# Kernel tuning notes

Measured on AMD Instinct MI355X. Metric: run time of the kernel, lower is better.

## Reference

```python
import jax, jax.numpy as jnp
import numpy as np

B, T, V, H = 16, 128, 32000, 768
P = H // 2
NBOW = 64
PAD = 0
EPS = 0.05     # label smoothing
TAU = 0.07
W_CE, W_AL, W_BOW, W_DIV, W_VAR = 1.0, 0.5, 0.2, 0.1, 0.05
BOW_IDS = jnp.arange(NBOW, dtype=jnp.int32) * 500  # registered buffer bow_indices_tensor


def _ln(x, g, b):
    m = jnp.mean(x, axis=-1, keepdims=True)
    v = jnp.mean((x - m) ** 2, axis=-1, keepdims=True)
    return (x - m) / jnp.sqrt(v + 1e-5) * g + b


def _l2norm(x):
    return x / jnp.maximum(jnp.linalg.norm(x, axis=-1, keepdims=True), 1e-12)


def _proj(x, g, bn, W1, b1, W2, b2):
    h = _ln(x, g, bn)
    h = jax.nn.gelu(h @ W1 + b1, approximate=False)  # torch nn.GELU default = exact
    return h @ W2 + b2


def setup_inputs() -> dict:
    key = jax.random.key(0)
    ks = jax.random.split(key, 12)
    s = 0.02
    return {
        "logits": jax.random.normal(ks[0], (B, T, V), dtype=jnp.float32),
        "labels": jax.random.randint(ks[1], (B, T), 0, V, dtype=jnp.int32),
        "attention_mask": jnp.ones((B, T), dtype=jnp.int32),
        "encoder_features": jax.random.normal(ks[2], (B, H), dtype=jnp.float32),
        "decoder_hidden": jax.random.normal(ks[3], (B, T, H), dtype=jnp.float32),
        "ln_g_e": jnp.ones((H,), jnp.float32), "ln_b_e": jnp.zeros((H,), jnp.float32),
        "W1_e": jax.random.normal(ks[4], (H, P), jnp.float32) * s, "b1_e": jnp.zeros((P,), jnp.float32),
        "W2_e": jax.random.normal(ks[5], (P, P), jnp.float32) * s, "b2_e": jnp.zeros((P,), jnp.float32),
        "ln_g_t": jnp.ones((H,), jnp.float32), "ln_b_t": jnp.zeros((H,), jnp.float32),
        "W1_t": jax.random.normal(ks[6], (H, P), jnp.float32) * s, "b1_t": jnp.zeros((P,), jnp.float32),
        "W2_t": jax.random.normal(ks[7], (P, P), jnp.float32) * s, "b2_t": jnp.zeros((P,), jnp.float32),
        "W_bow": jax.random.normal(ks[8], (H, NBOW), jnp.float32) * s, "b_bow": jnp.zeros((NBOW,), jnp.float32),
    }


def _forward(logits, labels, attention_mask, encoder_features, decoder_hidden,
             ln_g_e, ln_b_e, W1_e, b1_e, W2_e, b2_e,
             ln_g_t, ln_b_t, W1_t, b1_t, W2_t, b2_t,
             W_bow, b_bow):
    # --- label-smoothed CE over valid (non-pad, non -100) tokens ---
    valid = (labels != PAD) & (labels != -100)                      # (B,T)
    lab = jnp.clip(labels, 0, V - 1)
    lp = jax.nn.log_softmax(logits, axis=-1)                        # (B,T,V)
    lp_lab = jnp.take_along_axis(lp, lab[..., None], axis=-1)[..., 0]
    tok_loss = -((1.0 - EPS) * lp_lab + (EPS / V) * lp.sum(-1))     # smooth target = (1-eps) at label + eps/V everywhere
    vf = valid.astype(jnp.float32)
    ce = (tok_loss * vf).sum() / jnp.maximum(vf.sum(), 1.0)

    # --- contrastive alignment (InfoNCE both ways) ---
    m = attention_mask[..., None].astype(jnp.float32)               # (B,T,1)
    pooled = (decoder_hidden * m).sum(1) / jnp.maximum(m.sum(1), 1.0)
    z_e = _l2norm(_proj(encoder_features, ln_g_e, ln_b_e, W1_e, b1_e, W2_e, b2_e))
    z_t = _l2norm(_proj(pooled, ln_g_t, ln_b_t, W1_t, b1_t, W2_t, b2_t))
    sim = (z_e @ z_t.T) / TAU                                       # (B,B)
    li = -jnp.diag(jax.nn.log_softmax(sim, axis=-1)).mean()
    lj = -jnp.diag(jax.nn.log_softmax(sim.T, axis=-1)).mean()
    align = 0.5 * (li + lj)

    # --- BoW BCE: target[b,i] = any valid token of row b equals bow id i ---
    match = (lab[:, :, None] == BOW_IDS[None, None, :]) & valid[:, :, None]
    bow_t = match.any(axis=1).astype(jnp.float32)                   # (B,NBOW)
    bl = encoder_features @ W_bow + b_bow
    bce = jnp.mean(jnp.maximum(bl, 0.0) - bl * bow_t + jnp.log1p(jnp.exp(-jnp.abs(bl))))

    # --- diversity: mean |off-diagonal cosine sim| of encoder features ---
    nf = _l2norm(encoder_features)
    sm = nf @ nf.T
    off = 1.0 - jnp.eye(B, dtype=jnp.float32)
    div = (jnp.abs(sm) * off).sum() / (B * B - B)

    # --- variance: mean exp(-var_dim) (torch.var uses ddof=1) ---
    fvar = jnp.var(encoder_features, axis=0, ddof=1)
    var_l = jnp.mean(jnp.exp(-fvar))

    return W_CE * ce + W_AL * align + W_BOW * bce + W_DIV * div + W_VAR * var_l


def reference(logits, labels, attention_mask, encoder_features, decoder_hidden,
              ln_g_e, ln_b_e, W1_e, b1_e, W2_e, b2_e,
              ln_g_t, ln_b_t, W1_t, b1_t, W2_t, b2_t,
              W_bow, b_bow):
    return _forward(logits, labels, attention_mask, encoder_features, decoder_hidden,
                    ln_g_e, ln_b_e, W1_e, b1_e, W2_e, b2_e,
                    ln_g_t, ln_b_t, W1_t, b1_t, W2_t, b2_t,
                    W_bow, b_bow)
```

## Files before the change

### kernel.cpp

```cpp
#include <hip/hip_runtime.h>
#include <math.h>

#define BB 16
#define TT 128
#define VV 32000
#define HH 768
#define PP 384
#define NBOWD 64
#define EPS_LS 0.05f
#define TAUC 0.07f
#define SMALLB 101

__device__ __forceinline__ float blockReduceSum256(float v, float* sh) {
  int tid = threadIdx.x;
  sh[tid] = v;
  __syncthreads();
  for (int s = 128; s > 0; s >>= 1) {
    if (tid < s) sh[tid] += sh[tid + s];
    __syncthreads();
  }
  float r = sh[0];
  __syncthreads();
  return r;
}

__global__ __launch_bounds__(256) void fused_main(
    const float* __restrict__ logits, const int* __restrict__ labels, const int* __restrict__ amask,
    const float* __restrict__ enc, const float* __restrict__ dh,
    const float* __restrict__ g_e, const float* __restrict__ be_, const float* __restrict__ W1e,
    const float* __restrict__ b1e, const float* __restrict__ W2e, const float* __restrict__ b2e,
    const float* __restrict__ g_t, const float* __restrict__ bt_, const float* __restrict__ W1t,
    const float* __restrict__ b1t, const float* __restrict__ W2t, const float* __restrict__ b2t,
    const float* __restrict__ W_bow, const float* __restrict__ b_bow,
    float* __restrict__ tok, float* __restrict__ vfs,
    float* __restrict__ ze, float* __restrict__ zt,
    float* __restrict__ bowp, float* __restrict__ divp, float* __restrict__ var_p) {
  __shared__ float smem[1792];
  int tid = threadIdx.x;
  int blk = blockIdx.x;

  if (blk >= SMALLB) {
    int row = blk - SMALLB;
    const float* x = logits + (size_t)row * VV;
    const float4* x4 = (const float4*)x;
    float sa0 = 0.f, sa1 = 0.f, sa2 = 0.f, sa3 = 0.f;
    float ta0 = 0.f, ta1 = 0.f, ta2 = 0.f, ta3 = 0.f;
#pragma unroll
    for (int grp = 0; grp < 3; ++grp) {
      float4 v[8];
      const int base = (grp << 11) + tid;
#pragma unroll
      for (int u = 0; u < 8; ++u) v[u] = x4[base + (u << 8)];
#pragma unroll
      for (int u = 0; u < 8; ++u) {
        float4 w = v[u];
        float e = (__expf(w.x) + __expf(w.y)) + (__expf(w.z) + __expf(w.w));
        float q = (w.x + w.y) + (w.z + w.w);
        if ((u & 3) == 0) { sa0 += e; ta0 += q; }
        else if ((u & 3) == 1) { sa1 += e; ta1 += q; }
        else if ((u & 3) == 2) { sa2 += e; ta2 += q; }
        else { sa3 += e; ta3 += q; }
      }
    }
    {
      float4 v[7];
      const int base = 6144 + tid;
#pragma unroll
      for (int u = 0; u < 7; ++u) v[u] = x4[base + (u << 8)];
#pragma unroll
      for (int u = 0; u < 7; ++u) {
        float4 w = v[u];
        float e = (__expf(w.x) + __expf(w.y)) + (__expf(w.z) + __expf(w.w));
        float q = (w.x + w.y) + (w.z + w.w);
        if ((u & 3) == 0) { sa0 += e; ta0 += q; }
        else if ((u & 3) == 1) { sa1 += e; ta1 += q; }
        else if ((u & 3) == 2) { sa2 += e; ta2 += q; }
        else { sa3 += e; ta3 += q; }
      }
    }
    if (tid < 64) {
      float4 w = x4[7936 + tid];
      sa3 += (__expf(w.x) + __expf(w.y)) + (__expf(w.z) + __expf(w.w));
      ta3 += (w.x + w.y) + (w.z + w.w);
    }
    float s = (sa0 + sa1) + (sa2 + sa3);
    float sx = (ta0 + ta1) + (ta2 + ta3);

    float* ss_ = smem;
    float* sxa = smem + 256;
    ss_[tid] = s; sxa[tid] = sx;
    __syncthreads();
    for (int o = 128; o > 0; o >>= 1) {
      if (tid < o) {
        ss_[tid] += ss_[tid + o];
        sxa[tid] += sxa[tid + o];
      }
      __syncthreads();
    }
    if (tid == 0) {
      float L = logf(ss_[0]), SX = sxa[0];
      int lab = labels[row];
      bool valid = (lab != 0) && (lab != -100);
      int lc = lab < 0 ? 0 : (lab > VV - 1 ? VV - 1 : lab);
      float xl = x[lc];
      float lp_lab = xl - L;
      float lp_sum = SX - (float)VV * L;
      float tl = -((1.f - EPS_LS) * lp_lab + (EPS_LS / (float)VV) * lp_sum);
      tok[row] = valid ? tl : 0.f;
      vfs[row] = valid ? 1.f : 0.f;
    }
    return;
  }

  if (blk < 32) {
    float* xs = smem;
    float* hs = smem + 768;
    float* red = smem + 1152;
    float* mf = smem + 1408;
    float* mden = smem + 1536;
    bool is_t = blk >= BB;
    int b = blk & (BB - 1);
    const float *g, *bb_, *W1, *b1, *W2, *b2;
    float* zout;
    if (is_t) { g = g_t; bb_ = bt_; W1 = W1t; b1 = b1t; W2 = W2t; b2 = b2t; zout = zt; }
    else      { g = g_e; bb_ = be_; W1 = W1e; b1 = b1e; W2 = W2e; b2 = b2e; zout = ze; }

    if (is_t) {
      if (tid < TT) mf[tid] = (float)amask[b * TT + tid];
      __syncthreads();
      if (tid == 0) {
        float sum = 0.f;
        for (int t = 0; t < TT; t++) sum += mf[t];
        mden[0] = fmaxf(sum, 1.f);
      }
      __syncthreads();
      const float* dbase = dh + (size_t)b * TT * HH;
      for (int h = tid; h < HH; h += 256) {
        const float* db = dbase + h;
        float a0 = 0.f, a1 = 0.f, a2 = 0.f, a3 = 0.f;
#pragma unroll 8
        for (int t = 0; t < TT; t += 4) {
          a0 += db[(t + 0) * HH] * mf[t + 0];
          a1 += db[(t + 1) * HH] * mf[t + 1];
          a2 += db[(t + 2) * HH] * mf[t + 2];
          a3 += db[(t + 3) * HH] * mf[t + 3];
        }
        xs[h] = ((a0 + a1) + (a2 + a3)) / mden[0];
      }
    } else {
      for (int k = tid; k < HH; k += 256) xs[k] = enc[b * HH + k];
    }
    __syncthreads();

    float s1 = 0.f, s2 = 0.f;
    for (int k = tid; k < HH; k += 256) { float v = xs[k]; s1 += v; s2 += v * v; }
    s1 = blockReduceSum256(s1, red);
    s2 = blockReduceSum256(s2, red);
    float mean = s1 / (float)HH;
    float var = s2 / (float)HH - mean * mean;
    float rstd = rsqrtf(var + 1e-5f);
    for (int k = tid; k < HH; k += 256) xs[k] = (xs[k] - mean) * rstd * g[k] + bb_[k];
    __syncthreads();

    for (int j = tid; j < PP; j += 256) {
      float a0 = 0.f, a1 = 0.f;
#pragma unroll 8
      for (int k = 0; k < HH; k += 2) {
        a0 += xs[k] * W1[k * PP + j];
        a1 += xs[k + 1] * W1[(k + 1) * PP + j];
      }
      float acc = b1[j] + a0 + a1;
      hs[j] = 0.5f * acc * (1.f + erff(acc * 0.70710678118654752440f));
    }
    __syncthreads();
    for (int j = tid; j < PP; j += 256) {
      float a0 = 0.f, a1 = 0.f;
#pragma unroll 8
      for (int k = 0; k < PP; k += 2) {
        a0 += hs[k] * W2[k * PP + j];
        a1 += hs[k + 1] * W2[(k + 1) * PP + j];
      }
      xs[j] = b2[j] + a0 + a1;
    }
    __syncthreads();
    float sq = 0.f;
    for (int j = tid; j < PP; j += 256) { float v = xs[j]; sq += v * v; }
    sq = blockReduceSum256(sq, red);
    float inv = 1.f / fmaxf(sqrtf(sq), 1e-12f);
    for (int j = tid; j < PP; j += 256) zout[b * PP + j] = xs[j] * inv;
    return;
  }

  if (blk < 96) {
    int bb = blk - 32;
    int b = bb >> 2, kq = bb & 3;
    int iw = tid & 63, ks = tid >> 6;
    const float* er = enc + b * HH;
    int k0 = kq * 192 + ks * 48;
    float acc = 0.f;
#pragma unroll 8
    for (int k = 0; k < 48; ++k) acc += er[k0 + k] * W_bow[(k0 + k) * NBOWD + iw];
    smem[ks * 64 + iw] = acc;
    __syncthreads();
    if (tid < 64) bowp[bb * 64 + tid] = smem[tid] + smem[64 + tid] + smem[128 + tid] + smem[192 + tid];
    return;
  }

  if (blk < 100) {
    int kq = blk - 96;
    int i = tid >> 4, j = tid & 15;
    const float* a = enc + i * HH + kq * 192;
    const float* c = enc + j * HH + kq * 192;
    float a0 = 0.f, a1 = 0.f;
#pragma unroll 8
    for (int k = 0; k < 192; k += 2) {
      a0 += a[k] * c[k];
      a1 += a[k + 1] * c[k + 1];
    }
    divp[kq * 256 + tid] = a0 + a1;
    return;
  }

  {
    float vsum = 0.f;
    for (int d = tid; d < HH; d += 256) {
      float a1 = 0.f, a2 = 0.f;
#pragma unroll
      for (int b = 0; b < BB; b++) { float v = enc[b * HH + d]; a1 += v; a2 += v * v; }
      float mean = a1 / (float)BB;
      float vr = (a2 - (float)BB * mean * mean) / (float)(BB - 1);
      vsum += __expf(-vr);
    }
    float r = blockReduceSum256(vsum, smem);
    if (tid == 0) var_p[0] = r / (float)HH;
  }
}

__global__ __launch_bounds__(256) void finalize2(
    const float* __restrict__ tok, const float* __restrict__ vfs,
    const float* __restrict__ ze, const float* __restrict__ zt,
    const float* __restrict__ bowp, const float* __restrict__ divp, const float* __restrict__ var_p,
    const int* __restrict__ labels, const float* __restrict__ b_bow,
    float* __restrict__ out) {
  __shared__ float sh[256];
  __shared__ float smat[256];
  __shared__ float misc[40];
  __shared__ int flags[BB * NBOWD];
  int tid = threadIdx.x;

  for (int i = tid; i < BB * NBOWD; i += 256) flags[i] = 0;
  __syncthreads();
  for (int i = tid; i < BB * TT; i += 256) {
    int lab = labels[i];
    if (lab != 0 && lab != -100) {
      int lc = lab < 0 ? 0 : (lab > VV - 1 ? VV - 1 : lab);
      if (lc % 500 == 0) {
        int iw = lc / 500;
        if (iw < NBOWD) flags[(i >> 7) * NBOWD + iw] = 1;
      }
    }
  }

  float tsum = 0.f, csum = 0.f;
  for (int i = tid; i < BB * TT; i += 256) { tsum += tok[i]; csum += vfs[i]; }
  float ce_sum = blockReduceSum256(tsum, sh);
  float ce_cnt = blockReduceSum256(csum, sh);

  {
    int i = tid >> 4, j = tid & 15;
    const float* a = ze + i * PP;
    const float* c = zt + j * PP;
    float a0 = 0.f, a1 = 0.f;
#pragma unroll 8
    for (int k = 0; k < PP; k += 2) { a0 += a[k] * c[k]; a1 += a[k + 1] * c[k + 1]; }
    smat[tid] = (a0 + a1) * (1.f / TAUC);
  }
  __syncthreads();
  if (tid < 32) {
    bool isrow = tid < 16;
    int r = tid & 15;
    float mx = -1e30f;
    for (int j = 0; j < 16; j++) { float v = isrow ? smat[r * 16 + j] : smat[j * 16 + r]; mx = fmaxf(mx, v); }
    float se = 0.f;
    for (int j = 0; j < 16; j++) { float v = isrow ? smat[r * 16 + j] : smat[j * 16 + r]; se += __expf(v - mx); }
    misc[tid] = smat[r * 17] - mx - logf(se);
  }
  __syncthreads();
  float align;
  if (tid == 0) {
    float li = 0.f, lj = 0.f;
    for (int r = 0; r < 16; r++) { li += misc[r]; lj += misc[16 + r]; }
    misc[33] = 0.5f * (-(li / 16.f) - (lj / 16.f));
  }
  __syncthreads();
  align = misc[33];
  __syncthreads();

  float bsum = 0.f;
  for (int e = tid; e < BB * NBOWD; e += 256) {
    int b = e >> 6, iw = e & 63;
    float bl = b_bow[iw] + bowp[(b * 4 + 0) * 64 + iw] + bowp[(b * 4 + 1) * 64 + iw]
             + bowp[(b * 4 + 2) * 64 + iw] + bowp[(b * 4 + 3) * 64 + iw];
    float tgt = (float)flags[e];
    bsum += fmaxf(bl, 0.f) - bl * tgt + log1pf(__expf(-fabsf(bl)));
  }
  float bce = blockReduceSum256(bsum, sh) / (float)(BB * NBOWD);

  smat[tid] = divp[tid] + divp[256 + tid] + divp[512 + tid] + divp[768 + tid];
  __syncthreads();
  float contrib = 0.f;
  {
    int i = tid >> 4, j = tid & 15;
    if (i != j) {
      float ni = fmaxf(sqrtf(smat[i * 17]), 1e-12f);
      float nj = fmaxf(sqrtf(smat[j * 17]), 1e-12f);
      contrib = fabsf(smat[tid]) / (ni * nj);
    }
  }
  float divs = blockReduceSum256(contrib, sh) / (float)(BB * BB - BB);

  if (tid == 0) {
    float ce = ce_sum / fmaxf(ce_cnt, 1.f);
    out[0] = 1.0f * ce + 0.5f * align + 0.2f * bce + 0.1f * divs + 0.05f * var_p[0];
  }
}

extern "C" void kernel_launch(void* const* d_in, const int* in_sizes, int n_in,
                              void* d_out, int out_size, void* d_ws, size_t ws_size,
                              hipStream_t stream) {
  const float* logits = (const float*)d_in[0];
  const int* labels   = (const int*)d_in[1];
  const int* amask    = (const int*)d_in[2];
  const float* enc    = (const float*)d_in[3];
  const float* dh     = (const float*)d_in[4];
  const float* g_e    = (const float*)d_in[5];
  const float* be_    = (const float*)d_in[6];
  const float* W1e    = (const float*)d_in[7];
  const float* b1e    = (const float*)d_in[8];
  const float* W2e    = (const float*)d_in[9];
  const float* b2e    = (const float*)d_in[10];
  const float* g_t    = (const float*)d_in[11];
  const float* bt_    = (const float*)d_in[12];
  const float* W1t    = (const float*)d_in[13];
  const float* b1t    = (const float*)d_in[14];
  const float* W2t    = (const float*)d_in[15];
  const float* b2t    = (const float*)d_in[16];
  const float* W_bow  = (const float*)d_in[17];
  const float* b_bow  = (const float*)d_in[18];

  float* f     = (float*)d_ws;
  float* tok   = f;
  float* vfs   = f + 2048;
  float* ze    = f + 4096;
  float* zt    = f + 10240;
  float* bowp  = f + 16384;
  float* divp  = f + 20480;
  float* var_p = f + 21504;

  fused_main<<<SMALLB + BB * TT, 256, 0, stream>>>(
      logits, labels, amask, enc, dh,
      g_e, be_, W1e, b1e, W2e, b2e,
      g_t, bt_, W1t, b1t, W2t, b2t,
      W_bow, b_bow, tok, vfs, ze, zt, bowp, divp, var_p);
  finalize2<<<1, 256, 0, stream>>>(tok, vfs, ze, zt, bowp, divp, var_p, labels, b_bow, (float*)d_out);
}
```

Baseline: 480.6 us.

## Split decoder mean-pooling across blocks and move text projection to separate kernel

The masked mean-pool over decoder_hidden moves from 16 serial blocks (one per batch row, each also doing the full MLP) into 48 blocks, each pooling 256 hidden columns of one row. The text-side LayerNorm/MLP/normalize now runs in a new 16-block kernel launched after the main kernel. The aim is to shorten the critical-path tail block inside fused_main. The cost is an extra kernel launch and a round trip through global memory for the pooled features. Dot-product loops also get four accumulators instead of two.

```diff
diff --git a/kernel.cpp b/kernel.cpp
--- a/kernel.cpp
+++ b/kernel.cpp
@@ -9,7 +9,7 @@
 #define NBOWD 64
 #define EPS_LS 0.05f
 #define TAUC 0.07f
-#define SMALLB 101
+#define SMALLB 133
 
 __device__ __forceinline__ float blockReduceSum256(float v, float* sh) {
   int tid = threadIdx.x;
@@ -22,6 +22,53 @@
   float r = sh[0];
   __syncthreads();
   return r;
+}
+
+__device__ __forceinline__ void proj_tail(float* xs, float* hs, float* red,
+    const float* __restrict__ g, const float* __restrict__ bb_,
+    const float* __restrict__ W1, const float* __restrict__ b1,
+    const float* __restrict__ W2, const float* __restrict__ b2,
+    float* __restrict__ zrow, int tid) {
+  float s1 = 0.f, s2 = 0.f;
+  for (int k = tid; k < HH; k += 256) { float v = xs[k]; s1 += v; s2 += v * v; }
+  s1 = blockReduceSum256(s1, red);
+  s2 = blockReduceSum256(s2, red);
+  float mean = s1 / (float)HH;
+  float var = s2 / (float)HH - mean * mean;
+  float rstd = rsqrtf(var + 1e-5f);
+  for (int k = tid; k < HH; k += 256) xs[k] = (xs[k] - mean) * rstd * g[k] + bb_[k];
+  __syncthreads();
+
+  for (int j = tid; j < PP; j += 256) {
+    float a0 = 0.f, a1 = 0.f, a2 = 0.f, a3 = 0.f;
+#pragma unroll 8
+    for (int k = 0; k < HH; k += 4) {
+      a0 += xs[k]     * W1[(k)     * PP + j];
+      a1 += xs[k + 1] * W1[(k + 1) * PP + j];
+      a2 += xs[k + 2] * W1[(k + 2) * PP + j];
+      a3 += xs[k + 3] * W1[(k + 3) * PP + j];
+    }
+    float acc = b1[j] + (a0 + a1) + (a2 + a3);
+    hs[j] = 0.5f * acc * (1.f + erff(acc * 0.70710678118654752440f));
+  }
+  __syncthreads();
+  for (int j = tid; j < PP; j += 256) {
+    float a0 = 0.f, a1 = 0.f, a2 = 0.f, a3 = 0.f;
+#pragma unroll 8
+    for (int k = 0; k < PP; k += 4) {
+      a0 += hs[k]     * W2[(k)     * PP + j];
+      a1 += hs[k + 1] * W2[(k + 1) * PP + j];
+      a2 += hs[k + 2] * W2[(k + 2) * PP + j];
+      a3 += hs[k + 3] * W2[(k + 3) * PP + j];
+    }
+    xs[j] = b2[j] + (a0 + a1) + (a2 + a3);
+  }
+  __syncthreads();
+  float sq = 0.f;
+  for (int j = tid; j < PP; j += 256) { float v = xs[j]; sq += v * v; }
+  sq = blockReduceSum256(sq, red);
+  float inv = 1.f / fmaxf(sqrtf(sq), 1e-12f);
+  for (int j = tid; j < PP; j += 256) zrow[j] = xs[j] * inv;
 }
 
 __global__ __launch_bounds__(256) void fused_main(
@@ -29,13 +76,11 @@
     const float* __restrict__ enc, const float* __restrict__ dh,
     const float* __restrict__ g_e, const float* __restrict__ be_, const float* __restrict__ W1e,
     const float* __restrict__ b1e, const float* __restrict__ W2e, const float* __restrict__ b2e,
-    const float* __restrict__ g_t, const float* __restrict__ bt_, const float* __restrict__ W1t,
-    const float* __restrict__ b1t, const float* __restrict__ W2t, const float* __restrict__ b2t,
     const float* __restrict__ W_bow, const float* __restrict__ b_bow,
     float* __restrict__ tok, float* __restrict__ vfs,
-    float* __restrict__ ze, float* __restrict__ zt,
+    float* __restrict__ ze, float* __restrict__ pooled,
     float* __restrict__ bowp, float* __restrict__ divp, float* __restrict__ var_p) {
-  __shared__ float smem[1792];
+  __shared__ float smem[1408];
   int tid = threadIdx.x;
   int blk = blockIdx.x;
 
@@ -112,87 +157,43 @@
     return;
   }
 
-  if (blk < 32) {
+  if (blk < 16) {
     float* xs = smem;
     float* hs = smem + 768;
     float* red = smem + 1152;
-    float* mf = smem + 1408;
-    float* mden = smem + 1536;
-    bool is_t = blk >= BB;
-    int b = blk & (BB - 1);
-    const float *g, *bb_, *W1, *b1, *W2, *b2;
-    float* zout;
-    if (is_t) { g = g_t; bb_ = bt_; W1 = W1t; b1 = b1t; W2 = W2t; b2 = b2t; zout = zt; }
-    else      { g = g_e; bb_ = be_; W1 = W1e; b1 = b1e; W2 = W2e; b2 = b2e; zout = ze; }
-
-    if (is_t) {
-      if (tid < TT) mf[tid] = (float)amask[b * TT + tid];
-      __syncthreads();
-      if (tid == 0) {
-        float sum = 0.f;
-        for (int t = 0; t < TT; t++) sum += mf[t];
-        mden[0] = fmaxf(sum, 1.f);
-      }
-      __syncthreads();
-      const float* dbase = dh + (size_t)b * TT * HH;
-      for (int h = tid; h < HH; h += 256) {
-        const float* db = dbase + h;
-        float a0 = 0.f, a1 = 0.f, a2 = 0.f, a3 = 0.f;
-#pragma unroll 8
-        for (int t = 0; t < TT; t += 4) {
-          a0 += db[(t + 0) * HH] * mf[t + 0];
-          a1 += db[(t + 1) * HH] * mf[t + 1];
-          a2 += db[(t + 2) * HH] * mf[t + 2];
-          a3 += db[(t + 3) * HH] * mf[t + 3];
-        }
-        xs[h] = ((a0 + a1) + (a2 + a3)) / mden[0];
-      }
-    } else {
-      for (int k = tid; k < HH; k += 256) xs[k] = enc[b * HH + k];
-    }
-    __syncthreads();
-
-    float s1 = 0.f, s2 = 0.f;
-    for (int k = tid; k < HH; k += 256) { float v = xs[k]; s1 += v; s2 += v * v; }
-    s1 = blockReduceSum256(s1, red);
-    s2 = blockReduceSum256(s2, red);
-    float mean = s1 / (float)HH;
-    float var = s2 / (float)HH - mean * mean;
-    float rstd = rsqrtf(var + 1e-5f);
-    for (int k = tid; k < HH; k += 256) xs[k] = (xs[k] - mean) * rstd * g[k] + bb_[k];
-    __syncthreads();
-
-    for (int j = tid; j < PP; j += 256) {
-      float a0 = 0.f, a1 = 0.f;
-#pragma unroll 8
-      for (int k = 0; k < HH; k += 2) {
-        a0 += xs[k] * W1[k * PP + j];
-        a1 += xs[k + 1] * W1[(k + 1) * PP + j];
-      }
-      float acc = b1[j] + a0 + a1;
-      hs[j] = 0.5f * acc * (1.f + erff(acc * 0.70710678118654752440f));
-    }
-    __syncthreads();
-    for (int j = tid; j < PP; j += 256) {
-      float a0 = 0.f, a1 = 0.f;
-#pragma unroll 8
-      for (int k = 0; k < PP; k += 2) {
-        a0 += hs[k] * W2[k * PP + j];
-        a1 += hs[k + 1] * W2[(k + 1) * PP + j];
-      }
-      xs[j] = b2[j] + a0 + a1;
-    }
-    __syncthreads();
-    float sq = 0.f;
-    for (int j = tid; j < PP; j += 256) { float v = xs[j]; sq += v * v; }
-    sq = blockReduceSum256(sq, red);
-    float inv = 1.f / fmaxf(sqrtf(sq), 1e-12f);
-    for (int j = tid; j < PP; j += 256) zout[b * PP + j] = xs[j] * inv;
-    return;
-  }
-
-  if (blk < 96) {
-    int bb = blk - 32;
+    int b = blk;
+    for (int k = tid; k < HH; k += 256) xs[k] = enc[b * HH + k];
+    __syncthreads();
+    proj_tail(xs, hs, red, g_e, be_, W1e, b1e, W2e, b2e, ze + b * PP, tid);
+    return;
+  }
+
+  if (blk < 64) {
+    int bb = blk - 16;
+    int b = bb / 3, c = bb - 3 * b;
+    float* mf = smem;
+    if (tid < TT) mf[tid] = (float)amask[b * TT + tid];
+    __syncthreads();
+    int h = c * 256 + tid;
+    const float* db = dh + (size_t)b * TT * HH + h;
+    float a0 = 0.f, a1 = 0.f, a2 = 0.f, a3 = 0.f, a4 = 0.f, a5 = 0.f, a6 = 0.f, a7 = 0.f;
+#pragma unroll 2
+    for (int t = 0; t < TT; t += 8) {
+      a0 += db[(t + 0) * HH] * mf[t + 0];
+      a1 += db[(t + 1) * HH] * mf[t + 1];
+      a2 += db[(t + 2) * HH] * mf[t + 2];
+      a3 += db[(t + 3) * HH] * mf[t + 3];
+      a4 += db[(t + 4) * HH] * mf[t + 4];
+      a5 += db[(t + 5) * HH] * mf[t + 5];
+      a6 += db[(t + 6) * HH] * mf[t + 6];
+      a7 += db[(t + 7) * HH] * mf[t + 7];
+    }
+    pooled[b * HH + h] = ((a0 + a1) + (a2 + a3)) + ((a4 + a5) + (a6 + a7));
+    return;
+  }
+
+  if (blk < 128) {
+    int bb = blk - 64;
     int b = bb >> 2, kq = bb & 3;
     int iw = tid & 63, ks = tid >> 6;
     const float* er = enc + b * HH;
@@ -206,8 +207,8 @@
     return;
   }
 
-  if (blk < 100) {
-    int kq = blk - 96;
+  if (blk < 132) {
+    int kq = blk - 128;
     int i = tid >> 4, j = tid & 15;
     const float* a = enc + i * HH + kq * 192;
     const float* c = enc + j * HH + kq * 192;
@@ -234,6 +235,24 @@
     float r = blockReduceSum256(vsum, smem);
     if (tid == 0) var_p[0] = r / (float)HH;
   }
+}
+
+__global__ __launch_bounds__(256) void proj_t_kernel(
+    const float* __restrict__ pooled, const int* __restrict__ amask,
+    const float* __restrict__ g_t, const float* __restrict__ bt_,
+    const float* __restrict__ W1t, const float* __restrict__ b1t,
+    const float* __restrict__ W2t, const float* __restrict__ b2t,
+    float* __restrict__ zt) {
+  __shared__ float xs[HH];
+  __shared__ float hs[PP];
+  __shared__ float red[256];
+  int tid = threadIdx.x;
+  int b = blockIdx.x;
+  float msum = (tid < TT) ? (float)amask[b * TT + tid] : 0.f;
+  float mden = fmaxf(blockReduceSum256(msum, red), 1.f);
+  for (int k = tid; k < HH; k += 256) xs[k] = pooled[b * HH + k] / mden;
+  __syncthreads();
+  proj_tail(xs, hs, red, g_t, bt_, W1t, b1t, W2t, b2t, zt + b * PP, tid);
 }
 
 __global__ __launch_bounds__(256) void finalize2(
@@ -270,10 +289,13 @@
     int i = tid >> 4, j = tid & 15;
     const float* a = ze + i * PP;
     const float* c = zt + j * PP;
-    float a0 = 0.f, a1 = 0.f;
-#pragma unroll 8
-    for (int k = 0; k < PP; k += 2) { a0 += a[k] * c[k]; a1 += a[k + 1] * c[k + 1]; }
-    smat[tid] = (a0 + a1) * (1.f / TAUC);
+    float a0 = 0.f, a1 = 0.f, a2 = 0.f, a3 = 0.f;
+#pragma unroll 8
+    for (int k = 0; k < PP; k += 4) {
+      a0 += a[k] * c[k];     a1 += a[k + 1] * c[k + 1];
+      a2 += a[k + 2] * c[k + 2]; a3 += a[k + 3] * c[k + 3];
+    }
+    smat[tid] = ((a0 + a1) + (a2 + a3)) * (1.f / TAUC);
   }
   __syncthreads();
   if (tid < 32) {
@@ -348,19 +370,20 @@
   const float* W_bow  = (const float*)d_in[17];
   const float* b_bow  = (const float*)d_in[18];
 
-  float* f     = (float*)d_ws;
-  float* tok   = f;
-  float* vfs   = f + 2048;
-  float* ze    = f + 4096;
-  float* zt    = f + 10240;
-  float* bowp  = f + 16384;
-  float* divp  = f + 20480;
-  float* var_p = f + 21504;
+  float* f      = (float*)d_ws;
+  float* tok    = f;
+  float* vfs    = f + 2048;
+  float* ze     = f + 4096;
+  float* zt     = f + 10240;
+  float* bowp   = f + 16384;
+  float* divp   = f + 20480;
+  float* var_p  = f + 21504;
+  float* pooled = f + 21760;
 
   fused_main<<<SMALLB + BB * TT, 256, 0, stream>>>(
       logits, labels, amask, enc, dh,
       g_e, be_, W1e, b1e, W2e, b2e,
-      g_t, bt_, W1t, b1t, W2t, b2t,
-      W_bow, b_bow, tok, vfs, ze, zt, bowp, divp, var_p);
+      W_bow, b_bow, tok, vfs, ze, pooled, bowp, divp, var_p);
+  proj_t_kernel<<<BB, 256, 0, stream>>>(pooled, amask, g_t, bt_, W1t, b1t, W2t, b2t, zt);
   finalize2<<<1, 256, 0, stream>>>(tok, vfs, ze, zt, bowp, divp, var_p, labels, b_bow, (float*)d_out);
 }
```

New measurement: 501.1 us. 1.04x slower.
